# Optimization experiments

Measured on AMD Instinct MI355X. Metric: run time of the kernel, lower is better.

Reference implementation:

```python
import jax, jax.numpy as jnp
import numpy as np

B, T, F = 32, 512, 4096
H = 128            # num_lstm
NUM_CLASSES = 2    # dense outputs = NUM_CLASSES + 1 (CTC blank)


def setup_inputs() -> dict:
    key = jax.random.key(0)
    ks = jax.random.split(key, 6)
    x = jax.random.normal(ks[0], (B, T, F), dtype=jnp.float32)
    # Keras LSTM params: kernel [F, 4H], recurrent_kernel [H, 4H], bias [4H]
    # (gate order i, f, c, o). Glorot-ish scaling for stability.
    Wk = jax.random.normal(ks[1], (F, 4 * H), dtype=jnp.float32) / np.sqrt(F)
    Wr = jax.random.normal(ks[2], (H, 4 * H), dtype=jnp.float32) / np.sqrt(H)
    b = jnp.zeros((4 * H,), dtype=jnp.float32).at[H:2 * H].set(1.0)  # unit_forget_bias
    Wd = jax.random.normal(ks[3], (H, NUM_CLASSES + 1), dtype=jnp.float32) / np.sqrt(H)
    bd = jnp.zeros((NUM_CLASSES + 1,), dtype=jnp.float32)
    return {"x": x, "Wk": Wk, "Wr": Wr, "b": b, "Wd": Wd, "bd": bd}


def _lstm(x, Wk, Wr, b):
    # Precompute input projections for all timesteps (big GEMM once).
    z = jnp.einsum("btf,fg->btg", x, Wk) + b          # [B, T, 4H]
    z = jnp.transpose(z, (1, 0, 2))                    # [T, B, 4H]

    def step(carry, z_t):
        h, c = carry
        g = z_t + h @ Wr                               # [B, 4H]
        i = jax.nn.sigmoid(g[:, 0 * H:1 * H])
        f = jax.nn.sigmoid(g[:, 1 * H:2 * H])
        cc = jnp.tanh(g[:, 2 * H:3 * H])
        o = jax.nn.sigmoid(g[:, 3 * H:4 * H])
        c = f * c + i * cc
        h = o * jnp.tanh(c)
        return (h, c), h

    h0 = jnp.zeros((x.shape[0], H), dtype=x.dtype)
    c0 = jnp.zeros((x.shape[0], H), dtype=x.dtype)
    _, hs = jax.lax.scan(step, (h0, c0), z)            # hs: [T, B, H]
    return jnp.transpose(hs, (1, 0, 2))                # [B, T, H]


def reference(x, Wk, Wr, b, Wd, bd):
    # Inference-mode forward (dropout/recurrent_dropout inactive).
    h = _lstm(x, Wk, Wr, b)                            # [B, T, H]
    return h @ Wd + bd                                 # [B, T, num_classes+1]
```

## Files before the change

### kernel.cpp

```cpp
#include <hip/hip_runtime.h>
#include <hip/hip_bf16.h>
#include <hip/hip_fp16.h>
#include <math.h>

#define B_  32
#define T_  512
#define F_  4096
#define H_  128
#define G4H 512
#define NCLS 3
#define M_  (B_ * T_)
#define KSTEPS 128

typedef _Float16 f16x8 __attribute__((ext_vector_type(8)));
typedef _Float16 f16x4 __attribute__((ext_vector_type(4)));
typedef float    f32x4 __attribute__((ext_vector_type(4)));

__global__ __launch_bounds__(256) void cvt_wkT(
    const float* __restrict__ Wk, _Float16* __restrict__ btK)
{
    __shared__ float ls[64][65];
    const int k0 = blockIdx.x * 64;
    const int n0 = blockIdx.y * 64;
    const int tid = threadIdx.x;

    {
        int r  = tid >> 4;
        int c4 = (tid & 15) * 4;
        #pragma unroll
        for (int p = 0; p < 4; ++p) {
            float4 v = *reinterpret_cast<const float4*>(
                &Wk[(size_t)(k0 + r + p * 16) * G4H + n0 + c4]);
            ls[r + p * 16][c4 + 0] = v.x;
            ls[r + p * 16][c4 + 1] = v.y;
            ls[r + p * 16][c4 + 2] = v.z;
            ls[r + p * 16][c4 + 3] = v.w;
        }
    }
    __syncthreads();
    {
        int rn = tid >> 2;
        int ck = (tid & 3) * 16;
        f16x8 h0, h1;
        #pragma unroll
        for (int j = 0; j < 8; ++j) {
            h0[j] = (_Float16)ls[ck + j][rn];
            h1[j] = (_Float16)ls[ck + 8 + j][rn];
        }
        const int n    = n0 + rn;
        const int kg   = k0 + ck;
        const int kblk = kg >> 5;
        const int kk   = kg & 31;
        const int g0   = kk >> 3;
        const int sw   = (n >> 1) & 3;
        _Float16* base = btK + (size_t)kblk * (512 * 32) + (size_t)n * 32;
        *reinterpret_cast<f16x8*>(base + ((g0 ^ sw) << 3))       = h0;
        *reinterpret_cast<f16x8*>(base + (((g0 + 1) ^ sw) << 3)) = h1;
    }
}

__global__ __launch_bounds__(256) void cvt_wrT(
    const float* __restrict__ Wr, _Float16* __restrict__ wrT)
{
    __shared__ float ls[64][65];
    const int k0 = blockIdx.x * 64;
    const int n0 = blockIdx.y * 64;
    const int tid = threadIdx.x;
    {
        int r  = tid >> 4;
        int c4 = (tid & 15) * 4;
        #pragma unroll
        for (int p = 0; p < 4; ++p) {
            float4 v = *reinterpret_cast<const float4*>(
                &Wr[(size_t)(k0 + r + p * 16) * G4H + n0 + c4]);
            ls[r + p * 16][c4 + 0] = v.x;
            ls[r + p * 16][c4 + 1] = v.y;
            ls[r + p * 16][c4 + 2] = v.z;
            ls[r + p * 16][c4 + 3] = v.w;
        }
    }
    __syncthreads();
    {
        int rn = tid >> 2;
        int ck = (tid & 3) * 16;
        f16x8 h0, h1;
        #pragma unroll
        for (int j = 0; j < 8; ++j) {
            h0[j] = (_Float16)ls[ck + j][rn];
            h1[j] = (_Float16)ls[ck + 8 + j][rn];
        }
        _Float16* dst = &wrT[(size_t)(n0 + rn) * H_ + k0 + ck];
        *reinterpret_cast<f16x8*>(dst)     = h0;
        *reinterpret_cast<f16x8*>(dst + 8) = h1;
    }
}

__device__ __forceinline__ void lds_barrier() {
    asm volatile("s_waitcnt lgkmcnt(0)" ::: "memory");
    __builtin_amdgcn_s_barrier();
    asm volatile("" ::: "memory");
}

__global__ __launch_bounds__(512, 4) void gemm_fused(
    const float* __restrict__ x, const _Float16* __restrict__ btK,
    const float* __restrict__ bias, float* __restrict__ z)
{
    __shared__ __align__(16) _Float16 As[2][4][64 * 32];

    const int tid = threadIdx.x;
    const int w   = tid >> 6;
    const int l   = tid & 63;
    const int fr  = l & 15;
    const int q   = l >> 4;

    const int bid   = blockIdx.x;
    const int xcd   = bid & 7;
    const int idx   = bid >> 3;
    const int mt    = xcd * 32 + (idx >> 1);
    const int ntile = idx & 1;
    const int m0    = mt * 64;
    const int n0    = ntile * 256;

    const int ar = tid >> 3;
    const int hc = (tid & 7) * 4;
    const int abyte = ((((hc >> 3) ^ ((ar >> 1) & 3)) << 4) | ((hc << 1) & 15));
    const float* xrow = x + (size_t)(m0 + ar) * F_ + hc;

    const int nA = n0 + w * 32 + fr;
    const int nB = nA + 16;
    const _Float16* bp0 = btK + (size_t)nA * 32 + ((q ^ ((nA >> 1) & 3)) << 3);
    const _Float16* bp1 = btK + (size_t)nB * 32 + ((q ^ ((nB >> 1) & 3)) << 3);

    #define LOADB(t, bfv)                                                     \
    {                                                                         \
        bfv[0] = *reinterpret_cast<const f16x8*>(bp0 + (size_t)(t) * 16384);  \
        bfv[1] = *reinterpret_cast<const f16x8*>(bp1 + (size_t)(t) * 16384);  \
    }

    #define LOADX(t) (*reinterpret_cast<const float4*>(xrow + (size_t)(t) * 32))

    #define WRITE_A(v, G, s)                                                  \
    {                                                                         \
        f16x4 hh; hh[0] = (_Float16)v.x; hh[1] = (_Float16)v.y;               \
        hh[2] = (_Float16)v.z; hh[3] = (_Float16)v.w;                         \
        *reinterpret_cast<f16x4*>(                                            \
            reinterpret_cast<char*>(&As[G][s][0]) + ar * 64 + abyte) = hh;    \
    }

    #define COMPUTE(G, s, bfv)                                                \
    {                                                                         \
        f16x8 af[4];                                                          \
        _Pragma("unroll")                                                     \
        for (int i = 0; i < 4; ++i) {                                         \
            int r   = i * 16 + fr;                                            \
            int off = r * 64 + ((q ^ ((r >> 1) & 3)) << 4);                   \
            af[i] = *reinterpret_cast<const f16x8*>(                          \
                reinterpret_cast<const char*>(&As[G][s][0]) + off);           \
        }                                                                     \
        _Pragma("unroll")                                                     \
        for (int i = 0; i < 4; ++i)                                           \
            _Pragma("unroll")                                                 \
            for (int j = 0; j < 2; ++j)                                       \
                acc[i][j] = __builtin_amdgcn_mfma_f32_16x16x32_f16(           \
                    af[i], bfv[j], acc[i][j], 0, 0, 0);                       \
    }

    #define GROUP(t0, G)                                                      \
    {                                                                         \
        WRITE_A(xq0, G ^ 1, 0) WRITE_A(xq1, G ^ 1, 1)                         \
        WRITE_A(xq2, G ^ 1, 2) WRITE_A(xq3, G ^ 1, 3)                         \
        xq0 = LOADX((t0) + 8);  xq1 = LOADX((t0) + 9);                        \
        xq2 = LOADX((t0) + 10); xq3 = LOADX((t0) + 11);                       \
        COMPUTE(G, 0, bfA) LOADB((t0) + 2, bfA)                               \
        COMPUTE(G, 1, bfB) LOADB((t0) + 3, bfB)                               \
        COMPUTE(G, 2, bfA) LOADB((t0) + 4, bfA)                               \
        COMPUTE(G, 3, bfB) LOADB((t0) + 5, bfB)                               \
        lds_barrier();                                                        \
    }

    f32x4 acc[4][2] = {};
    f16x8 bfA[2], bfB[2];
    float4 xq0, xq1, xq2, xq3;

    xq0 = LOADX(0); xq1 = LOADX(1); xq2 = LOADX(2); xq3 = LOADX(3);
    WRITE_A(xq0, 0, 0) WRITE_A(xq1, 0, 1) WRITE_A(xq2, 0, 2) WRITE_A(xq3, 0, 3)
    xq0 = LOADX(4); xq1 = LOADX(5); xq2 = LOADX(6); xq3 = LOADX(7);
    LOADB(0, bfA) LOADB(1, bfB)
    lds_barrier();

    for (int gg = 0; gg < 30; gg += 2) {
        const int t0 = gg * 4;
        GROUP(t0, 0)
        GROUP(t0 + 4, 1)
    }
    {
        WRITE_A(xq0, 1, 0) WRITE_A(xq1, 1, 1) WRITE_A(xq2, 1, 2) WRITE_A(xq3, 1, 3)
        COMPUTE(0, 0, bfA) LOADB(122, bfA)
        COMPUTE(0, 1, bfB) LOADB(123, bfB)
        COMPUTE(0, 2, bfA) LOADB(124, bfA)
        COMPUTE(0, 3, bfB) LOADB(125, bfB)
        lds_barrier();
    }
    {
        COMPUTE(1, 0, bfA) LOADB(126, bfA)
        COMPUTE(1, 1, bfB) LOADB(127, bfB)
        COMPUTE(1, 2, bfA)
        COMPUTE(1, 3, bfB)
    }

    #undef LOADB
    #undef LOADX
    #undef WRITE_A
    #undef COMPUTE
    #undef GROUP

    #pragma unroll
    for (int j = 0; j < 2; ++j) {
        const int nn = n0 + w * 32 + j * 16 + fr;
        const float bj = bias[nn];
        #pragma unroll
        for (int i = 0; i < 4; ++i)
            #pragma unroll
            for (int r = 0; r < 4; ++r)
                z[(size_t)(m0 + i * 16 + q * 4 + r) * G4H + nn]
                    = acc[i][j][r] + bj;
    }
}

__device__ __forceinline__ float sig_f(float x) {
    return __builtin_amdgcn_rcpf(
        1.0f + __builtin_amdgcn_exp2f(-1.442695040888963f * x));
}
__device__ __forceinline__ float tanh_f(float x) {
    return 1.0f - 2.0f * __builtin_amdgcn_rcpf(
        1.0f + __builtin_amdgcn_exp2f(2.885390081777927f * x));
}

__global__ __launch_bounds__(512, 2) void lstm_mfma(
    const float* __restrict__ z,
    const _Float16* __restrict__ wrT,
    float* __restrict__ hs,
    float* __restrict__ cst,
    _Float16* __restrict__ h16,
    int t0)
{
    const int b    = blockIdx.x;
    const int tid  = threadIdx.x;
    const int w    = tid >> 6;
    const int lane = tid & 63;
    const int l15  = lane & 15;
    const int q    = lane >> 4;
    const int jj   = w * 16 + l15;

    __shared__ __align__(16) _Float16 hA[2][128];

    f16x8 bf[4][4];
    #pragma unroll
    for (int g = 0; g < 4; ++g)
        #pragma unroll
        for (int kf = 0; kf < 4; ++kf)
            bf[g][kf] = *reinterpret_cast<const f16x8*>(
                &wrT[(size_t)(g * H_ + jj) * H_ + kf * 32 + q * 8]);

    float cstate;
    if (t0 == 0) {
        if (tid < 128) reinterpret_cast<unsigned int*>(hA)[tid] = 0u;
        cstate = 0.f;
    } else {
        if (tid < 64)
            reinterpret_cast<unsigned int*>(hA[0])[tid] =
                reinterpret_cast<const unsigned int*>(h16 + (size_t)b * H_)[tid];
        cstate = cst[(size_t)b * H_ + jj];
    }

    const float* zq    = z  + (size_t)b * T_ * G4H + jj;
    float*       hbase = hs + (size_t)b * T_ * H_;

    const f32x4 zero4 = {0.f, 0.f, 0.f, 0.f};

    #define LOADZ(t, d)                                                       \
    {                                                                         \
        int zo = (((t) & (T_ - 1)) << 9);                                     \
        d.x = zq[zo];       d.y = zq[zo + 128];                               \
        d.z = zq[zo + 256]; d.w = zq[zo + 384];                               \
    }

    float4 zP0, zP1, zP2, zP3;
    LOADZ(t0 + 0, zP0) LOADZ(t0 + 1, zP1)
    LOADZ(t0 + 2, zP2) LOADZ(t0 + 3, zP3)

    __syncthreads();

    #define LSTM_STEP(t, CUR, ZZ)                                             \
    {                                                                         \
        f16x8 af0 = *reinterpret_cast<const f16x8*>(&hA[CUR][0 * 32 + q * 8]);\
        f16x8 af1 = *reinterpret_cast<const f16x8*>(&hA[CUR][1 * 32 + q * 8]);\
        f16x8 af2 = *reinterpret_cast<const f16x8*>(&hA[CUR][2 * 32 + q * 8]);\
        f16x8 af3 = *reinterpret_cast<const f16x8*>(&hA[CUR][3 * 32 + q * 8]);\
        float zt0_ = ZZ.x, zt1_ = ZZ.y, zt2_ = ZZ.z, zt3_ = ZZ.w;             \
        LOADZ((t) + 4, ZZ)                                                    \
        float gv[4];                                                          \
        _Pragma("unroll")                                                     \
        for (int g = 0; g < 4; ++g) {                                         \
            f32x4 aA = __builtin_amdgcn_mfma_f32_16x16x32_f16(                \
                af0, bf[g][0], zero4, 0, 0, 0);                               \
            aA = __builtin_amdgcn_mfma_f32_16x16x32_f16(                      \
                af1, bf[g][1], aA, 0, 0, 0);                                  \
            f32x4 aB = __builtin_amdgcn_mfma_f32_16x16x32_f16(                \
                af2, bf[g][2], zero4, 0, 0, 0);                               \
            aB = __builtin_amdgcn_mfma_f32_16x16x32_f16(                      \
                af3, bf[g][3], aB, 0, 0, 0);                                  \
            gv[g] = aA[0] + aB[0];                                            \
        }                                                                     \
        float iv = sig_f(gv[0] + zt0_);                                       \
        float fv = sig_f(gv[1] + zt1_);                                       \
        float cc = tanh_f(gv[2] + zt2_);                                      \
        float ov = sig_f(gv[3] + zt3_);                                       \
        cstate = fv * cstate + iv * cc;                                       \
        float h = ov * tanh_f(cstate);                                        \
        if (q == 0) {                                                         \
            hA[CUR ^ 1][jj] = (_Float16)h;                                    \
            hbase[((t) << 7) + jj] = h;                                       \
        }                                                                     \
        lds_barrier();                                                        \
    }

    for (int t = t0; t < t0 + 256; t += 4) {
        LSTM_STEP(t,     0, zP0)
        LSTM_STEP(t + 1, 1, zP1)
        LSTM_STEP(t + 2, 0, zP2)
        LSTM_STEP(t + 3, 1, zP3)
    }
    #undef LSTM_STEP
    #undef LOADZ

    if (q == 0) cst[(size_t)b * H_ + jj] = cstate;
    if (tid < 64)
        reinterpret_cast<unsigned int*>(h16 + (size_t)b * H_)[tid] =
            reinterpret_cast<unsigned int*>(hA[0])[tid];
}

__global__ __launch_bounds__(256) void dense_out(
    const float* __restrict__ hs, const float* __restrict__ Wd,
    const float* __restrict__ bd, float* __restrict__ out)
{
    int idx = blockIdx.x * 256 + threadIdx.x;
    if (idx >= B_ * T_ * NCLS) return;
    int cls = idx % NCLS;
    int row = idx / NCLS;
    const float* h = hs + (size_t)row * H_;
    float acc = bd[cls];
    #pragma unroll 8
    for (int k = 0; k < H_; ++k) acc += h[k] * Wd[k * NCLS + cls];
    out[idx] = acc;
}

extern "C" void kernel_launch(void* const* d_in, const int* in_sizes, int n_in,
                              void* d_out, int out_size, void* d_ws, size_t ws_size,
                              hipStream_t stream)
{
    const float* x  = (const float*)d_in[0];
    const float* Wk = (const float*)d_in[1];
    const float* Wr = (const float*)d_in[2];
    const float* b  = (const float*)d_in[3];
    const float* Wd = (const float*)d_in[4];
    const float* bd = (const float*)d_in[5];
    float* out = (float*)d_out;

    float*     z   = (float*)d_ws;
    float*     hs  = z + (size_t)M_ * G4H;
    _Float16*  btK = (_Float16*)(hs + (size_t)M_ * H_);
    _Float16*  wrT = btK + (size_t)G4H * F_;
    float*     cst = (float*)(wrT + (size_t)G4H * H_);
    _Float16*  h16 = (_Float16*)(cst + (size_t)B_ * H_);

    cvt_wkT<<<dim3(F_ / 64, G4H / 64), 256, 0, stream>>>(Wk, btK);
    cvt_wrT<<<dim3(H_ / 64, G4H / 64), 256, 0, stream>>>(Wr, wrT);
    gemm_fused<<<512, 512, 0, stream>>>(x, btK, b, z);
    lstm_mfma<<<B_, 512, 0, stream>>>(z, wrT, hs, cst, h16, 0);
    lstm_mfma<<<B_, 512, 0, stream>>>(z, wrT, hs, cst, h16, 256);
    int total = B_ * T_ * NCLS;
    dense_out<<<(total + 255) / 256, 256, 0, stream>>>(hs, Wd, bd, out);
}
```

Before: 357.5 us.

## Fuse input GEMM and LSTM recurrence into one persistent kernel with flag sync

```diff
diff --git a/kernel.cpp b/kernel.cpp
--- a/kernel.cpp
+++ b/kernel.cpp
@@ -60,12 +60,14 @@
 }
 
 __global__ __launch_bounds__(256) void cvt_wrT(
-    const float* __restrict__ Wr, _Float16* __restrict__ wrT)
+    const float* __restrict__ Wr, _Float16* __restrict__ wrT,
+    unsigned int* __restrict__ flags)
 {
     __shared__ float ls[64][65];
     const int k0 = blockIdx.x * 64;
     const int n0 = blockIdx.y * 64;
     const int tid = threadIdx.x;
+    if (blockIdx.x == 0 && blockIdx.y == 0 && tid < 128) flags[tid] = 0u;
     {
         int r  = tid >> 4;
         int c4 = (tid & 15) * 4;
@@ -101,6 +103,281 @@
     asm volatile("" ::: "memory");
 }
 
+__device__ __forceinline__ float tanh_f(float x) {
+    return 1.0f - 2.0f * __builtin_amdgcn_rcpf(
+        1.0f + __builtin_amdgcn_exp2f(2.885390081777927f * x));
+}
+__device__ __forceinline__ float sig_f(float x) {
+    return __builtin_amdgcn_rcpf(
+        1.0f + __builtin_amdgcn_exp2f(-1.442695040888963f * x));
+}
+
+__device__ __forceinline__ void wait4(unsigned int* f) {
+    while (__hip_atomic_load(f, __ATOMIC_ACQUIRE, __HIP_MEMORY_SCOPE_AGENT) < 4u)
+        __builtin_amdgcn_s_sleep(2);
+}
+
+__global__ __launch_bounds__(1024) void fused_overlap(
+    const float* __restrict__ x, const _Float16* __restrict__ btK,
+    const float* __restrict__ bias, float* __restrict__ zA,
+    float* __restrict__ zB, const _Float16* __restrict__ wrT,
+    float* __restrict__ hs, unsigned int* __restrict__ flags)
+{
+    float pv[32];
+    #pragma unroll
+    for (int i = 0; i < 32; ++i)
+        asm volatile("v_mov_b32 %0, %1" : "=v"(pv[i]) : "v"((float)i));
+
+    __shared__ __align__(16) char smem[65536];
+    const int tid = threadIdx.x;
+    const int bid = blockIdx.x;
+
+    if (bid >= 32) {
+        const int lt = tid & 511;
+        const int vb = tid >> 9;
+        const int w  = lt >> 6;
+        const int l  = lt & 63;
+        const int fr = l & 15;
+        const int q  = l >> 4;
+
+        const int ar = lt >> 3;
+        const int hc = (lt & 7) * 4;
+        const int abyte = ((((hc >> 3) ^ ((ar >> 1) & 3)) << 4) | ((hc << 1) & 15));
+
+        char* AsB = smem + vb * 32768;
+
+        for (int it = bid - 32; it < 512; it += 224) {
+            const int s  = it >> 7;
+            const int r  = it & 127;
+            const int b  = r >> 2;
+            const int nh = (r >> 1) & 1;
+            const int kh = r & 1;
+            const int m0 = b * T_ + s * 128 + vb * 64;
+            const int n0 = nh * 256;
+            const int kb = kh * 64;
+
+            const float* xrow = x + (size_t)(m0 + ar) * F_ + hc;
+            const int nA = n0 + w * 32 + fr;
+            const int nB = nA + 16;
+            const _Float16* bp0 = btK + (size_t)nA * 32 + ((q ^ ((nA >> 1) & 3)) << 3);
+            const _Float16* bp1 = btK + (size_t)nB * 32 + ((q ^ ((nB >> 1) & 3)) << 3);
+
+            #define LOADB(t, bfv)                                             \
+            {                                                                 \
+                bfv[0] = *reinterpret_cast<const f16x8*>(bp0 + (size_t)(t) * 16384); \
+                bfv[1] = *reinterpret_cast<const f16x8*>(bp1 + (size_t)(t) * 16384); \
+            }
+            #define LOADX(t) (*reinterpret_cast<const float4*>(xrow + (size_t)(t) * 32))
+            #define WRITE_A(v, G, ss)                                         \
+            {                                                                 \
+                f16x4 hh; hh[0] = (_Float16)v.x; hh[1] = (_Float16)v.y;       \
+                hh[2] = (_Float16)v.z; hh[3] = (_Float16)v.w;                 \
+                *reinterpret_cast<f16x4*>(                                    \
+                    AsB + ((G) * 4 + (ss)) * 4096 + ar * 64 + abyte) = hh;    \
+            }
+            #define COMPUTE(G, ss, bfv)                                       \
+            {                                                                 \
+                f16x8 af[4];                                                  \
+                _Pragma("unroll")                                             \
+                for (int i = 0; i < 4; ++i) {                                 \
+                    int rr  = i * 16 + fr;                                    \
+                    int off = rr * 64 + ((q ^ ((rr >> 1) & 3)) << 4);         \
+                    af[i] = *reinterpret_cast<const f16x8*>(                  \
+                        AsB + ((G) * 4 + (ss)) * 4096 + off);                 \
+                }                                                             \
+                _Pragma("unroll")                                             \
+                for (int i = 0; i < 4; ++i)                                   \
+                    _Pragma("unroll")                                         \
+                    for (int j = 0; j < 2; ++j)                               \
+                        acc[i][j] = __builtin_amdgcn_mfma_f32_16x16x32_f16(   \
+                            af[i], bfv[j], acc[i][j], 0, 0, 0);               \
+            }
+            #define GROUP(t0, G)                                              \
+            {                                                                 \
+                WRITE_A(xq0, G ^ 1, 0) WRITE_A(xq1, G ^ 1, 1)                 \
+                WRITE_A(xq2, G ^ 1, 2) WRITE_A(xq3, G ^ 1, 3)                 \
+                xq0 = LOADX((t0) + 8);  xq1 = LOADX((t0) + 9);                \
+                xq2 = LOADX((t0) + 10); xq3 = LOADX((t0) + 11);               \
+                COMPUTE(G, 0, bfA) LOADB((t0) + 2, bfA)                       \
+                COMPUTE(G, 1, bfB) LOADB((t0) + 3, bfB)                       \
+                COMPUTE(G, 2, bfA) LOADB((t0) + 4, bfA)                       \
+                COMPUTE(G, 3, bfB) LOADB((t0) + 5, bfB)                       \
+                lds_barrier();                                                \
+            }
+
+            f32x4 acc[4][2] = {};
+            f16x8 bfA[2], bfB[2];
+            float4 xq0, xq1, xq2, xq3;
+
+            xq0 = LOADX(kb + 0); xq1 = LOADX(kb + 1);
+            xq2 = LOADX(kb + 2); xq3 = LOADX(kb + 3);
+            WRITE_A(xq0, 0, 0) WRITE_A(xq1, 0, 1)
+            WRITE_A(xq2, 0, 2) WRITE_A(xq3, 0, 3)
+            xq0 = LOADX(kb + 4); xq1 = LOADX(kb + 5);
+            xq2 = LOADX(kb + 6); xq3 = LOADX(kb + 7);
+            LOADB(kb, bfA) LOADB(kb + 1, bfB)
+            lds_barrier();
+
+            for (int gg = 0; gg < 14; gg += 2) {
+                const int t0 = kb + gg * 4;
+                GROUP(t0, 0)
+                GROUP(t0 + 4, 1)
+            }
+            {
+                WRITE_A(xq0, 1, 0) WRITE_A(xq1, 1, 1)
+                WRITE_A(xq2, 1, 2) WRITE_A(xq3, 1, 3)
+                COMPUTE(0, 0, bfA) LOADB(kb + 58, bfA)
+                COMPUTE(0, 1, bfB) LOADB(kb + 59, bfB)
+                COMPUTE(0, 2, bfA) LOADB(kb + 60, bfA)
+                COMPUTE(0, 3, bfB) LOADB(kb + 61, bfB)
+                lds_barrier();
+            }
+            {
+                COMPUTE(1, 0, bfA) LOADB(kb + 62, bfA)
+                COMPUTE(1, 1, bfB) LOADB(kb + 63, bfB)
+                COMPUTE(1, 2, bfA)
+                COMPUTE(1, 3, bfB)
+            }
+            #undef LOADB
+            #undef LOADX
+            #undef WRITE_A
+            #undef COMPUTE
+            #undef GROUP
+
+            float* zt = kh ? zB : zA;
+            #pragma unroll
+            for (int j = 0; j < 2; ++j) {
+                const int nn = n0 + w * 32 + j * 16 + fr;
+                const float bj = kh ? bias[nn] : 0.0f;
+                #pragma unroll
+                for (int i = 0; i < 4; ++i)
+                    #pragma unroll
+                    for (int rr = 0; rr < 4; ++rr)
+                        zt[(size_t)(m0 + i * 16 + q * 4 + rr) * G4H + nn]
+                            = acc[i][j][rr] + bj;
+            }
+
+            __threadfence();
+            __syncthreads();
+            if (tid == 0)
+                __hip_atomic_fetch_add(&flags[(b << 2) + s], 1u,
+                                       __ATOMIC_RELEASE, __HIP_MEMORY_SCOPE_AGENT);
+            __syncthreads();
+        }
+    } else {
+        const int b    = bid;
+        const int lt   = tid;
+        const int w    = (lt >> 6) & 7;
+        const int lane = lt & 63;
+        const int l15  = lane & 15;
+        const int q    = lane >> 4;
+        const int jj   = w * 16 + l15;
+
+        _Float16 (*hA)[128] = reinterpret_cast<_Float16(*)[128]>(smem);
+
+        f16x8 bf[4][4];
+        float cstate = 0.f;
+        const float* zqA = zA + (size_t)b * T_ * G4H + jj;
+        const float* zqB = zB + (size_t)b * T_ * G4H + jj;
+        float*     hbase = hs + (size_t)b * T_ * H_;
+        const f32x4 zero4 = {0.f, 0.f, 0.f, 0.f};
+
+        if (tid < 512) {
+            #pragma unroll
+            for (int g = 0; g < 4; ++g)
+                #pragma unroll
+                for (int kf = 0; kf < 4; ++kf)
+                    bf[g][kf] = *reinterpret_cast<const f16x8*>(
+                        &wrT[(size_t)(g * H_ + jj) * H_ + kf * 32 + q * 8]);
+            if (tid < 128) reinterpret_cast<unsigned int*>(hA)[tid] = 0u;
+        }
+
+        if (tid == 0) wait4(&flags[b << 2]);
+        __syncthreads();
+
+        #define LOADZ(t, d)                                                   \
+        {                                                                     \
+            int zo = (((t) & (T_ - 1)) << 9);                                 \
+            d.x = zqA[zo]       + zqB[zo];                                    \
+            d.y = zqA[zo + 128] + zqB[zo + 128];                              \
+            d.z = zqA[zo + 256] + zqB[zo + 256];                              \
+            d.w = zqA[zo + 384] + zqB[zo + 384];                              \
+        }
+
+        float4 zP0, zP1, zP2, zP3;
+        if (tid < 512) {
+            LOADZ(0, zP0) LOADZ(1, zP1) LOADZ(2, zP2) LOADZ(3, zP3)
+        }
+        __syncthreads();
+
+        #define FSTEP(t, CUR, ZZ)                                             \
+        {                                                                     \
+            if (tid < 512) {                                                  \
+                f16x8 af0 = *reinterpret_cast<const f16x8*>(&hA[CUR][0 * 32 + q * 8]); \
+                f16x8 af1 = *reinterpret_cast<const f16x8*>(&hA[CUR][1 * 32 + q * 8]); \
+                f16x8 af2 = *reinterpret_cast<const f16x8*>(&hA[CUR][2 * 32 + q * 8]); \
+                f16x8 af3 = *reinterpret_cast<const f16x8*>(&hA[CUR][3 * 32 + q * 8]); \
+                float zt0_ = ZZ.x, zt1_ = ZZ.y, zt2_ = ZZ.z, zt3_ = ZZ.w;     \
+                LOADZ((t) + 4, ZZ)                                            \
+                float gv[4];                                                  \
+                _Pragma("unroll")                                             \
+                for (int g = 0; g < 4; ++g) {                                 \
+                    f32x4 aA = __builtin_amdgcn_mfma_f32_16x16x32_f16(        \
+                        af0, bf[g][0], zero4, 0, 0, 0);                       \
+                    aA = __builtin_amdgcn_mfma_f32_16x16x32_f16(              \
+                        af1, bf[g][1], aA, 0, 0, 0);                          \
+                    f32x4 aB = __builtin_amdgcn_mfma_f32_16x16x32_f16(        \
+                        af2, bf[g][2], zero4, 0, 0, 0);                       \
+                    aB = __builtin_amdgcn_mfma_f32_16x16x32_f16(              \
+                        af3, bf[g][3], aB, 0, 0, 0);                          \
+                    gv[g] = aA[0] + aB[0];                                    \
+                }                                                             \
+                float iv = sig_f(gv[0] + zt0_);                               \
+                float fv = sig_f(gv[1] + zt1_);                               \
+                float cc = tanh_f(gv[2] + zt2_);                              \
+                float ov = sig_f(gv[3] + zt3_);                               \
+                cstate = fv * cstate + iv * cc;                               \
+                float h = ov * tanh_f(cstate);                                \
+                if (q == 0) {                                                 \
+                    hA[CUR ^ 1][jj] = (_Float16)h;                            \
+                    hbase[((t) << 7) + jj] = h;                               \
+                }                                                             \
+            }                                                                 \
+            lds_barrier();                                                    \
+        }
+
+        for (int s8 = 0; s8 < 4; ++s8) {
+            const int tb = s8 * 128;
+            for (int tq = 0; tq < 124; tq += 4) {
+                FSTEP(tb + tq + 0, 0, zP0)
+                FSTEP(tb + tq + 1, 1, zP1)
+                FSTEP(tb + tq + 2, 0, zP2)
+                FSTEP(tb + tq + 3, 1, zP3)
+            }
+            if (s8 < 3) {
+                if (tid == 0) wait4(&flags[(b << 2) + s8 + 1]);
+                __syncthreads();
+            }
+            FSTEP(tb + 124, 0, zP0)
+            FSTEP(tb + 125, 1, zP1)
+            FSTEP(tb + 126, 0, zP2)
+            FSTEP(tb + 127, 1, zP3)
+        }
+        #undef FSTEP
+        #undef LOADZ
+    }
+
+    asm volatile("" ::
+        "v"(pv[0]),  "v"(pv[1]),  "v"(pv[2]),  "v"(pv[3]),
+        "v"(pv[4]),  "v"(pv[5]),  "v"(pv[6]),  "v"(pv[7]),
+        "v"(pv[8]),  "v"(pv[9]),  "v"(pv[10]), "v"(pv[11]),
+        "v"(pv[12]), "v"(pv[13]), "v"(pv[14]), "v"(pv[15]),
+        "v"(pv[16]), "v"(pv[17]), "v"(pv[18]), "v"(pv[19]),
+        "v"(pv[20]), "v"(pv[21]), "v"(pv[22]), "v"(pv[23]),
+        "v"(pv[24]), "v"(pv[25]), "v"(pv[26]), "v"(pv[27]),
+        "v"(pv[28]), "v"(pv[29]), "v"(pv[30]), "v"(pv[31]));
+}
+
 __global__ __launch_bounds__(512, 4) void gemm_fused(
     const float* __restrict__ x, const _Float16* __restrict__ btK,
     const float* __restrict__ bias, float* __restrict__ z)
@@ -136,9 +413,7 @@
         bfv[0] = *reinterpret_cast<const f16x8*>(bp0 + (size_t)(t) * 16384);  \
         bfv[1] = *reinterpret_cast<const f16x8*>(bp1 + (size_t)(t) * 16384);  \
     }
-
     #define LOADX(t) (*reinterpret_cast<const float4*>(xrow + (size_t)(t) * 32))
-
     #define WRITE_A(v, G, s)                                                  \
     {                                                                         \
         f16x4 hh; hh[0] = (_Float16)v.x; hh[1] = (_Float16)v.y;               \
@@ -146,7 +421,6 @@
         *reinterpret_cast<f16x4*>(                                            \
             reinterpret_cast<char*>(&As[G][s][0]) + ar * 64 + abyte) = hh;    \
     }
-
     #define COMPUTE(G, s, bfv)                                                \
     {                                                                         \
         f16x8 af[4];                                                          \
@@ -164,7 +438,6 @@
                 acc[i][j] = __builtin_amdgcn_mfma_f32_16x16x32_f16(           \
                     af[i], bfv[j], acc[i][j], 0, 0, 0);                       \
     }
-
     #define GROUP(t0, G)                                                      \
     {                                                                         \
         WRITE_A(xq0, G ^ 1, 0) WRITE_A(xq1, G ^ 1, 1)                         \
@@ -207,7 +480,6 @@
         COMPUTE(1, 2, bfA)
         COMPUTE(1, 3, bfB)
     }
-
     #undef LOADB
     #undef LOADX
     #undef WRITE_A
@@ -227,22 +499,10 @@
     }
 }
 
-__device__ __forceinline__ float sig_f(float x) {
-    return __builtin_amdgcn_rcpf(
-        1.0f + __builtin_amdgcn_exp2f(-1.442695040888963f * x));
-}
-__device__ __forceinline__ float tanh_f(float x) {
-    return 1.0f - 2.0f * __builtin_amdgcn_rcpf(
-        1.0f + __builtin_amdgcn_exp2f(2.885390081777927f * x));
-}
-
 __global__ __launch_bounds__(512, 2) void lstm_mfma(
-    const float* __restrict__ z,
-    const _Float16* __restrict__ wrT,
-    float* __restrict__ hs,
-    float* __restrict__ cst,
-    _Float16* __restrict__ h16,
-    int t0)
+    const float* __restrict__ z, const _Float16* __restrict__ wrT,
+    float* __restrict__ hs, float* __restrict__ cst,
+    _Float16* __restrict__ h16, int t0)
 {
     const int b    = blockIdx.x;
     const int tid  = threadIdx.x;
@@ -275,7 +535,6 @@
 
     const float* zq    = z  + (size_t)b * T_ * G4H + jj;
     float*       hbase = hs + (size_t)b * T_ * H_;
-
     const f32x4 zero4 = {0.f, 0.f, 0.f, 0.f};
 
     #define LOADZ(t, d)                                                       \
@@ -367,18 +626,40 @@
     const float* bd = (const float*)d_in[5];
     float* out = (float*)d_out;
 
-    float*     z   = (float*)d_ws;
-    float*     hs  = z + (size_t)M_ * G4H;
-    _Float16*  btK = (_Float16*)(hs + (size_t)M_ * H_);
-    _Float16*  wrT = btK + (size_t)G4H * F_;
-    float*     cst = (float*)(wrT + (size_t)G4H * H_);
-    _Float16*  h16 = (_Float16*)(cst + (size_t)B_ * H_);
-
-    cvt_wkT<<<dim3(F_ / 64, G4H / 64), 256, 0, stream>>>(Wk, btK);
-    cvt_wrT<<<dim3(H_ / 64, G4H / 64), 256, 0, stream>>>(Wr, wrT);
-    gemm_fused<<<512, 512, 0, stream>>>(x, btK, b, z);
-    lstm_mfma<<<B_, 512, 0, stream>>>(z, wrT, hs, cst, h16, 0);
-    lstm_mfma<<<B_, 512, 0, stream>>>(z, wrT, hs, cst, h16, 256);
-    int total = B_ * T_ * NCLS;
-    dense_out<<<(total + 255) / 256, 256, 0, stream>>>(hs, Wd, bd, out);
-}
+    const size_t zElems  = (size_t)M_ * G4H;
+    const size_t hsElems = (size_t)M_ * H_;
+    const size_t need_ov = (2 * zElems + hsElems) * 4 +
+                           (size_t)G4H * F_ * 2 + (size_t)G4H * H_ * 2 +
+                           128 * 4 + 256;
+
+    if (ws_size >= need_ov) {
+        float*        zA    = (float*)d_ws;
+        float*        zB    = zA + zElems;
+        float*        hs    = zB + zElems;
+        _Float16*     btK   = (_Float16*)(hs + hsElems);
+        _Float16*     wrT   = btK + (size_t)G4H * F_;
+        unsigned int* flags = (unsigned int*)(wrT + (size_t)G4H * H_);
+
+        cvt_wkT<<<dim3(F_ / 64, G4H / 64), 256, 0, stream>>>(Wk, btK);
+        cvt_wrT<<<dim3(H_ / 64, G4H / 64), 256, 0, stream>>>(Wr, wrT, flags);
+        fused_overlap<<<256, 1024, 0, stream>>>(x, btK, b, zA, zB, wrT, hs, flags);
+        int total = B_ * T_ * NCLS;
+        dense_out<<<(total + 255) / 256, 256, 0, stream>>>(hs, Wd, bd, out);
+    } else {
+        float*        z     = (float*)d_ws;
+        float*        hs    = z + zElems;
+        _Float16*     btK   = (_Float16*)(hs + hsElems);
+        _Float16*     wrT   = btK + (size_t)G4H * F_;
+        float*        cst   = (float*)(wrT + (size_t)G4H * H_);
+        _Float16*     h16   = (_Float16*)(cst + (size_t)B_ * H_);
+        unsigned int* flags = (unsigned int*)(h16 + (size_t)B_ * H_);
+
+        cvt_wkT<<<dim3(F_ / 64, G4H / 64), 256, 0, stream>>>(Wk, btK);
+        cvt_wrT<<<dim3(H_ / 64, G4H / 64), 256, 0, stream>>>(Wr, wrT, flags);
+        gemm_fused<<<512, 512, 0, stream>>>(x, btK, b, z);
+        lstm_mfma<<<B_, 512, 0, stream>>>(z, wrT, hs, cst, h16, 0);
+        lstm_mfma<<<B_, 512, 0, stream>>>(z, wrT, hs, cst, h16, 256);
+        int total = B_ * T_ * NCLS;
+        dense_out<<<(total + 255) / 256, 256, 0, stream>>>(hs, Wd, bd, out);
+    }
+}
```

After: 843.9 us. +136.1%, slower.
